# Kernel optimization log

Hardware: AMD Instinct MI355X
Metric: run time of the kernel (lower is better)

## Reference

```python
import jax, jax.numpy as jnp
import numpy as np

H = 4          # attention heads
NEG_SLOPE = 0.2

def _gat_layer(h, src, dst, W, a_src, a_dst, b):
    # h: [N, F_in]; W: [F_in, H*D]; a_src/a_dst: [H, D]; b: [D]
    N = h.shape[0]
    D = a_src.shape[1]
    xh = (h @ W).reshape(N, H, D)                       # [N,H,D]
    al_src = jnp.einsum('nhd,hd->nh', xh, a_src)        # [N,H]
    al_dst = jnp.einsum('nhd,hd->nh', xh, a_dst)        # [N,H]
    e = jax.nn.leaky_relu(al_src[src] + al_dst[dst], NEG_SLOPE)  # [E,H]
    # segment softmax over incoming edges of each destination node
    m = jax.ops.segment_max(e, dst, num_segments=N)     # [N,H]
    ex = jnp.exp(e - m[dst])
    s = jax.ops.segment_sum(ex, dst, num_segments=N)
    alpha = ex / (s[dst] + 1e-16)                       # [E,H]
    out = jax.ops.segment_sum(xh[src] * alpha[:, :, None], dst, num_segments=N)  # [N,H,D]
    return out.mean(axis=1) + b                         # concat=False -> mean heads


def setup_inputs() -> dict:
    key = jax.random.key(0)
    ks = jax.random.split(key, 16)
    N, E, F_in, Dh = 50000, 400000, 128, 128
    inp = {
        'x': jax.random.normal(ks[0], (N, F_in), jnp.float32),
        'edge_index': jax.random.randint(ks[1], (2, E), 0, N, jnp.int64),
    }
    def glorot(k, shape):
        fan = shape[0] + shape[-1]
        return jax.random.uniform(k, shape, jnp.float32, -1.0, 1.0) * np.sqrt(6.0 / fan)
    dims = [F_in, Dh, Dh]
    for i, fin in enumerate(dims, start=1):
        inp[f'W{i}'] = glorot(ks[2 + 4 * i], (fin, H * Dh))
        inp[f'a_src{i}'] = glorot(ks[3 + 4 * i], (H, Dh))
        inp[f'a_dst{i}'] = glorot(ks[4 + 4 * i], (H, Dh))
        inp[f'b{i}'] = jnp.zeros((Dh,), jnp.float32)
    inp['Wp'] = glorot(ks[2], (Dh, Dh))
    inp['bp'] = jnp.zeros((Dh,), jnp.float32)
    return inp


def reference(x, edge_index, W1, a_src1, a_dst1, b1, W2, a_src2, a_dst2, b2,
              W3, a_src3, a_dst3, b3, Wp, bp):
    N = x.shape[0]
    loops = jnp.arange(N, dtype=edge_index.dtype)
    src = jnp.concatenate([edge_index[0], loops])   # GATConv adds self-loops
    dst = jnp.concatenate([edge_index[1], loops])
    h = x
    for W, a_s, a_d, b in ((W1, a_src1, a_dst1, b1),
                           (W2, a_src2, a_dst2, b2),
                           (W3, a_src3, a_dst3, b3)):
        h = _gat_layer(h, src, dst, W, a_s, a_d, b)
        h = jax.nn.relu(h)   # dropout is identity in eval mode
    return h @ Wp + bp
```

## Files before the change

### kernel.cpp

```cpp
#include <hip/hip_runtime.h>
#include <cstddef>
#include <cstdint>

typedef _Float16 half8 __attribute__((ext_vector_type(8)));
typedef float f32x4 __attribute__((ext_vector_type(4)));
typedef float f32x2 __attribute__((ext_vector_type(2)));
typedef unsigned short ushort_t;
typedef unsigned int uint_t;
typedef ushort_t ushort4v __attribute__((ext_vector_type(4)));
typedef float f32x4v __attribute__((ext_vector_type(4)));

#define INV_LN2 1.4426950408889634f

__device__ __forceinline__ ushort_t f_to_f16(float f) {
  _Float16 h = (_Float16)f;
  union { _Float16 h; ushort_t u; } v; v.h = h; return v.u;
}
__device__ __forceinline__ float f16_to_f(ushort_t u) {
  union { ushort_t u; _Float16 h; } v; v.u = u; return (float)v.h;
}

__global__ __launch_bounds__(64) void detect_i64_kernel(const int* __restrict__ ei,
                                                        int* __restrict__ flag) {
  if (threadIdx.x == 0) {
    int is32 = 0;
    for (int i = 1; i < 1001; i += 2) {
      if (ei[i] != 0) { is32 = 1; break; }
    }
    *flag = is32;
  }
}

__device__ __forceinline__ int load_src(const int* ei, int is32, int E, int e) {
  return is32 ? ei[e] : ei[2 * e];
}
__device__ __forceinline__ int load_dst(const int* ei, int is32, int E, int e) {
  return is32 ? ei[E + e] : ei[2 * (E + e)];
}

__global__ __launch_bounds__(256) void deg_kernel(const int* __restrict__ ei,
                                                  const int* __restrict__ flag,
                                                  int E, int N, int* __restrict__ deg) {
  int e = blockIdx.x * 256 + threadIdx.x;
  if (e >= E + N) return;
  int d = (e < E) ? load_dst(ei, *flag, E, e) : (e - E);
  atomicAdd(&deg[d], 1);
}

__global__ __launch_bounds__(256) void scan_blk_kernel(const int* __restrict__ deg,
                                                       int* __restrict__ rowptr,
                                                       int* __restrict__ bsum, int N) {
  __shared__ int buf[256];
  int b = blockIdx.x, t = threadIdx.x, i = b * 256 + t;
  int v = (i < N) ? deg[i] : 0;
  buf[t] = v;
  __syncthreads();
  for (int off = 1; off < 256; off <<= 1) {
    int add = (t >= off) ? buf[t - off] : 0;
    __syncthreads();
    buf[t] += add;
    __syncthreads();
  }
  if (i < N) rowptr[i + 1] = buf[t];
  if (t == 255) bsum[b] = buf[255];
  if (b == 0 && t == 0) rowptr[0] = 0;
}

__global__ __launch_bounds__(256) void scan_top_kernel(int* __restrict__ bsum, int NB) {
  __shared__ int buf[256];
  int t = threadIdx.x;
  int v = (t < NB) ? bsum[t] : 0;
  buf[t] = v;
  __syncthreads();
  for (int off = 1; off < 256; off <<= 1) {
    int add = (t >= off) ? buf[t - off] : 0;
    __syncthreads();
    buf[t] += add;
    __syncthreads();
  }
  if (t < NB) bsum[t] = buf[t];
}

__global__ __launch_bounds__(256) void scan_add_kernel(int* __restrict__ rowptr,
                                                       const int* __restrict__ bsum, int N) {
  int b = blockIdx.x, t = threadIdx.x, i = b * 256 + t;
  if (b > 0 && i < N) rowptr[i + 1] += bsum[b - 1];
}

__global__ __launch_bounds__(256) void fill_kernel(const int* __restrict__ ei,
                                                   const int* __restrict__ flag,
                                                   int E, int N,
                                                   const int* __restrict__ rowptr,
                                                   int* __restrict__ fillc,
                                                   int* __restrict__ colbuf) {
  int e = blockIdx.x * 256 + threadIdx.x;
  if (e >= E + N) return;
  int s, d;
  if (e < E) { int is32 = *flag; s = load_src(ei, is32, E, e); d = load_dst(ei, is32, E, e); }
  else { s = e - E; d = s; }
  int pos = atomicAdd(&fillc[d], 1);
  colbuf[rowptr[d] + pos] = s;
}

__global__ __launch_bounds__(256) void split_x16_kernel(const float* __restrict__ h,
                                                        ushort_t* __restrict__ h16,
                                                        int n) {
  int i = (blockIdx.x * 256 + threadIdx.x) * 4;
  if (i >= n) return;
  f32x4v v = *(const f32x4v*)&h[i];
  ushort4v s;
  s[0] = f_to_f16(v[0]); s[1] = f_to_f16(v[1]);
  s[2] = f_to_f16(v[2]); s[3] = f_to_f16(v[3]);
  *(ushort4v*)&h16[i] = s;
}

__global__ __launch_bounds__(256) void split_wt_frag_kernel(const float* __restrict__ W,
                                                            ushort_t* __restrict__ Wf) {
  int t = blockIdx.x * 256 + threadIdx.x;
  int blk = t >> 7, rem = t & 127;
  int c16 = blk >> 4, k8 = blk & 15;
  int cl = rem >> 3, kl = rem & 7;
  int col = c16 * 16 + cl, k = k8 * 8 + kl;
  Wf[t] = f_to_f16(W[(size_t)k * 128 + col]);
}

__global__ __launch_bounds__(256) void split_wstack_frag_kernel(const float* __restrict__ W,
                                                                ushort_t* __restrict__ Wf) {
  int t = blockIdx.x * 256 + threadIdx.x;
  int c16 = t >> 13;
  int r = t & 8191;
  int k8 = r >> 7;
  int rem = r & 127;
  int rl = rem >> 3, kl = rem & 7;
  int col = c16 * 16 + rl;
  int k = k8 * 8 + kl;
  int h = k >> 7, f = k & 127;
  Wf[t] = f_to_f16(0.25f * W[(size_t)f * 512 + h * 128 + col]);
}

__global__ __launch_bounds__(256) void wsd_kernel(const float* __restrict__ W,
                                                  const float* __restrict__ a_src,
                                                  const float* __restrict__ a_dst,
                                                  float* __restrict__ Ws4,
                                                  float* __restrict__ Wd4,
                                                  float* __restrict__ Wsh,
                                                  float* __restrict__ Wdh) {
  int wave = threadIdx.x >> 6, lane = threadIdx.x & 63;
  int f = blockIdx.x * 4 + wave;
  int base = lane * 8;
  float4 w0 = *(const float4*)&W[(size_t)f * 512 + base];
  float4 w1 = *(const float4*)&W[(size_t)f * 512 + base + 4];
  float4 s0 = *(const float4*)&a_src[base];
  float4 s1 = *(const float4*)&a_src[base + 4];
  float4 d0 = *(const float4*)&a_dst[base];
  float4 d1 = *(const float4*)&a_dst[base + 4];
  float ps = w0.x*s0.x + w0.y*s0.y + w0.z*s0.z + w0.w*s0.w
           + w1.x*s1.x + w1.y*s1.y + w1.z*s1.z + w1.w*s1.w;
  float pd = w0.x*d0.x + w0.y*d0.y + w0.z*d0.z + w0.w*d0.w
           + w1.x*d1.x + w1.y*d1.y + w1.z*d1.z + w1.w*d1.w;
#pragma unroll
  for (int off = 1; off <= 8; off <<= 1) {
    ps += __shfl_xor(ps, off);
    pd += __shfl_xor(pd, off);
  }
  if ((lane & 15) == 0) {
    int h = lane >> 4;
    float vs = ps * INV_LN2, vd = pd * INV_LN2;
    Ws4[f * 4 + h] = vs;
    Wd4[f * 4 + h] = vd;
    Wsh[h * 128 + f] = vs;
    Wdh[h * 128 + f] = vd;
  }
}

__global__ __launch_bounds__(256) void al_x_kernel(const float* __restrict__ x,
                                                   const float* __restrict__ Wsh,
                                                   const float* __restrict__ Wdh,
                                                   float* __restrict__ al_src,
                                                   float* __restrict__ al_dst, int N) {
  __shared__ float sWs[512], sWd[512];
  int t = threadIdx.x;
  sWs[t] = Wsh[t]; sWs[t + 256] = Wsh[t + 256];
  sWd[t] = Wdh[t]; sWd[t + 256] = Wdh[t + 256];
  __syncthreads();
  int wave = t >> 6, lane = t & 63;
  int n = blockIdx.x * 4 + wave;
  if (n >= N) return;
  float2 hv = *(const float2*)&x[(size_t)n * 128 + lane * 2];
  float p[8];
#pragma unroll
  for (int hh = 0; hh < 4; ++hh) {
    p[hh]     = hv.x * sWs[hh * 128 + 2 * lane] + hv.y * sWs[hh * 128 + 2 * lane + 1];
    p[4 + hh] = hv.x * sWd[hh * 128 + 2 * lane] + hv.y * sWd[hh * 128 + 2 * lane + 1];
  }
#pragma unroll
  for (int off = 32; off; off >>= 1)
#pragma unroll
    for (int i = 0; i < 8; ++i) p[i] += __shfl_xor(p[i], off);
  if (lane == 0) {
#pragma unroll
    for (int hh = 0; hh < 4; ++hh) {
      al_src[n * 4 + hh] = p[hh];
      al_dst[n * 4 + hh] = p[4 + hh];
    }
  }
}

__global__ __launch_bounds__(256) void agg_G_kernel(const ushort_t* __restrict__ h16,
                                                    const float* __restrict__ al_src,
                                                    const float* __restrict__ al_dst,
                                                    const int* __restrict__ rowptr,
                                                    const int* __restrict__ colbuf,
                                                    ushort_t* __restrict__ Gf, int N) {
  int wave = threadIdx.x >> 6, lane = threadIdx.x & 63;
  int hl = lane & 31;
  int half_base = lane & 32;
  int q = hl >> 2, hc = hl & 3;
  int qb = lane & ~3;
  int n = blockIdx.x * 8 + wave * 2 + (lane >> 5);
  bool alive = n < N;
  int beg = 0, d = 0;
  float ald_hc = 0.f;
  if (alive) {
    beg = rowptr[n];
    d = rowptr[n + 1] - beg;
    ald_hc = al_dst[(size_t)n * 4 + hc];
  }
  int dm1 = max(d - 1, 0);
  float m_run = -1e30f;
  f32x2 ss01 = {0.f, 0.f}, ss23 = {0.f, 0.f};
  f32x2 a0a = {0.f,0.f}, a0b = {0.f,0.f};
  f32x2 a1a = {0.f,0.f}, a1b = {0.f,0.f};
  f32x2 a2a = {0.f,0.f}, a2b = {0.f,0.f};
  f32x2 a3a = {0.f,0.f}, a3b = {0.f,0.f};

  for (int c0 = 0; c0 < d; c0 += 8) {
    int cn = min(8, d - c0);
    int j = c0 + q;
    int sq = colbuf[beg + min(j, dm1)];
    float e = al_src[(size_t)sq * 4 + hc] + ald_hc;
    e = fmaxf(e, 0.2f * e);
    e = (q < cn) ? e : -1e30f;
    float mc = e;
    mc = fmaxf(mc, __shfl_xor(mc, 4));
    mc = fmaxf(mc, __shfl_xor(mc, 8));
    mc = fmaxf(mc, __shfl_xor(mc, 16));
    float nm = fmaxf(m_run, mc);
    float fown = exp2f(m_run - nm);
    m_run = nm;
    float w_own = (q < cn) ? exp2f(e - nm) : 0.f;
    float f0 = __shfl(fown, qb + 0), f1 = __shfl(fown, qb + 1);
    float f2 = __shfl(fown, qb + 2), f3 = __shfl(fown, qb + 3);
    ss01 *= f32x2{f0, f1}; ss23 *= f32x2{f2, f3};
    f32x2 F0 = {f0, f0}, F1 = {f1, f1}, F2 = {f2, f2}, F3 = {f3, f3};
    a0a *= F0; a0b *= F0; a1a *= F1; a1b *= F1;
    a2a *= F2; a2b *= F2; a3a *= F3; a3b *= F3;
    int s_c = __shfl(sq, half_base);
    ushort4v hv_c = *(const ushort4v*)&h16[(size_t)s_c * 128 + hl * 4];
    for (int jj = 0; jj < cn; ++jj) {
      int s_n = __shfl(sq, half_base + min(jj + 1, cn - 1) * 4);
      ushort4v hv_n = *(const ushort4v*)&h16[(size_t)s_n * 128 + hl * 4];
      int wb = half_base + jj * 4;
      float w0 = __shfl(w_own, wb + 0);
      float w1 = __shfl(w_own, wb + 1);
      float w2 = __shfl(w_own, wb + 2);
      float w3 = __shfl(w_own, wb + 3);
      ss01 += f32x2{w0, w1}; ss23 += f32x2{w2, w3};
      f32x2 v01 = {f16_to_f(hv_c[0]), f16_to_f(hv_c[1])};
      f32x2 v23 = {f16_to_f(hv_c[2]), f16_to_f(hv_c[3])};
      a0a += f32x2{w0, w0} * v01; a0b += f32x2{w0, w0} * v23;
      a1a += f32x2{w1, w1} * v01; a1b += f32x2{w1, w1} * v23;
      a2a += f32x2{w2, w2} * v01; a2b += f32x2{w2, w2} * v23;
      a3a += f32x2{w3, w3} * v01; a3b += f32x2{w3, w3} * v23;
      hv_c = hv_n;
    }
  }
  if (!alive) return;
  float g[4][4];
  float inv;
  inv = 1.f / (ss01.x + 1e-16f);
  g[0][0] = a0a.x * inv; g[0][1] = a0a.y * inv; g[0][2] = a0b.x * inv; g[0][3] = a0b.y * inv;
  inv = 1.f / (ss01.y + 1e-16f);
  g[1][0] = a1a.x * inv; g[1][1] = a1a.y * inv; g[1][2] = a1b.x * inv; g[1][3] = a1b.y * inv;
  inv = 1.f / (ss23.x + 1e-16f);
  g[2][0] = a2a.x * inv; g[2][1] = a2a.y * inv; g[2][2] = a2b.x * inv; g[2][3] = a2b.y * inv;
  inv = 1.f / (ss23.y + 1e-16f);
  g[3][0] = a3a.x * inv; g[3][1] = a3a.y * inv; g[3][2] = a3b.x * inv; g[3][3] = a3b.y * inv;
#pragma unroll
  for (int h = 0; h < 4; ++h) {
    ushort_t q0 = f_to_f16(g[h][0]), q1 = f_to_f16(g[h][1]);
    ushort_t q2 = f_to_f16(g[h][2]), q3 = f_to_f16(g[h][3]);
    size_t o = ((size_t)(n >> 4) * 64 + h * 16 + (hl >> 1)) * 128 + (n & 15) * 8 + (hl & 1) * 4;
    *(uint2*)&Gf[o] = make_uint2((uint_t)q0 | ((uint_t)q1 << 16),
                                 (uint_t)q2 | ((uint_t)q3 << 16));
  }
}

template <int K, int MODE>
__global__ __launch_bounds__(256) void gemm_frag_kernel(
    const ushort_t* __restrict__ Af, const ushort_t* __restrict__ Bf,
    ushort_t* __restrict__ H16, ushort_t* __restrict__ Cf16, float* __restrict__ Cf,
    const float* __restrict__ WsN, const float* __restrict__ WdN,
    float* __restrict__ alS, float* __restrict__ alD,
    int M, const float* __restrict__ bias) {
  constexpr int KT = K >> 5;
  constexpr int PS = 16 * K;
  int lane = threadIdx.x & 63;
  int wid = blockIdx.x * 4 + (threadIdx.x >> 6);
  int krow = lane >> 4, ml = lane & 15;
  int lb = krow * 128 + ml * 8;
  size_t abase = (size_t)wid * PS + lb;
  f32x4 acc[8] = {};
  half8 a_c = *(const half8*)&Af[abase];
#pragma unroll
  for (int kt = 0; kt < KT; ++kt) {
    half8 a_n = a_c;
    if (kt + 1 < KT) a_n = *(const half8*)&Af[abase + (kt + 1) * 512];
    half8 b[8];
#pragma unroll
    for (int j = 0; j < 8; ++j)
      b[j] = *(const half8*)&Bf[j * PS + kt * 512 + lb];
#pragma unroll
    for (int j = 0; j < 8; ++j)
      acc[j] = __builtin_amdgcn_mfma_f32_16x16x32_f16(a_c, b[j], acc[j], 0, 0, 0);
    a_c = a_n;
  }
  int wrow0 = wid * 16;
  if (MODE == 0) {
    float ps[4][4] = {};
    float pd[4][4] = {};
#pragma unroll
    for (int j = 0; j < 8; ++j) {
      int col = j * 16 + ml;
      float bv = bias[col];
      float4 w4s = *(const float4*)&WsN[col * 4];
      float4 w4d = *(const float4*)&WdN[col * 4];
#pragma unroll
      for (int r = 0; r < 4; ++r) {
        int row = wrow0 + krow * 4 + r;
        float v = fmaxf(acc[j][r] + bv, 0.f);
        if (row < M) H16[(size_t)row * 128 + col] = f_to_f16(v);
        ps[0][r] += v * w4s.x; ps[1][r] += v * w4s.y;
        ps[2][r] += v * w4s.z; ps[3][r] += v * w4s.w;
        pd[0][r] += v * w4d.x; pd[1][r] += v * w4d.y;
        pd[2][r] += v * w4d.z; pd[3][r] += v * w4d.w;
      }
    }
#pragma unroll
    for (int off = 1; off <= 8; off <<= 1) {
#pragma unroll
      for (int hh = 0; hh < 4; ++hh)
#pragma unroll
        for (int r = 0; r < 4; ++r) {
          ps[hh][r] += __shfl_xor(ps[hh][r], off);
          pd[hh][r] += __shfl_xor(pd[hh][r], off);
        }
    }
    if (ml == 0) {
#pragma unroll
      for (int r = 0; r < 4; ++r) {
        int row = wrow0 + krow * 4 + r;
        if (row < M) {
#pragma unroll
          for (int hh = 0; hh < 4; ++hh) {
            alS[row * 4 + hh] = ps[hh][r];
            alD[row * 4 + hh] = pd[hh][r];
          }
        }
      }
    }
  } else {
#pragma unroll
    for (int j = 0; j < 8; ++j) {
      int col = j * 16 + ml;
      float bv = bias[col];
#pragma unroll
      for (int r = 0; r < 4; ++r) {
        int row = wrow0 + krow * 4 + r;
        if (row < M) {
          float v = acc[j][r] + bv;
          if (MODE != 2) v = fmaxf(v, 0.f);
          if (MODE == 1) {
            size_t o = ((size_t)(row >> 4) * 16 + (col >> 3)) * 128 + (row & 15) * 8 + (col & 7);
            Cf16[o] = f_to_f16(v);
          } else {
            Cf[(size_t)row * 128 + col] = v;
          }
        }
      }
    }
  }
}

extern "C" void kernel_launch(void* const* d_in, const int* in_sizes, int n_in,
                              void* d_out, int out_size, void* d_ws, size_t ws_size,
                              hipStream_t stream) {
  const float* x  = (const float*)d_in[0];
  const int*   ei = (const int*)d_in[1];
  const float* Wl[3]  = {(const float*)d_in[2], (const float*)d_in[6], (const float*)d_in[10]};
  const float* asr[3] = {(const float*)d_in[3], (const float*)d_in[7], (const float*)d_in[11]};
  const float* adr[3] = {(const float*)d_in[4], (const float*)d_in[8], (const float*)d_in[12]};
  const float* bl[3]  = {(const float*)d_in[5], (const float*)d_in[9], (const float*)d_in[13]};
  const float* Wp = (const float*)d_in[14];
  const float* bp = (const float*)d_in[15];

  const int N = in_sizes[0] / 128;
  const int E = in_sizes[1] / 2;
  const int EN = E + N;
  const int Mtiles = (N + 127) / 128;
  const int Mp = Mtiles * 128;
  const int NB = (N + 255) / 256;
  const int NPB = Mp / 16 / 4;

  char* ws = (char*)d_ws;
  size_t off = 0;
  auto carve = [&](size_t bytes) -> void* {
    void* p = ws + off;
    off = (off + bytes + 255) & ~(size_t)255;
    return p;
  };
  ushort_t* Gf    = (ushort_t*)carve((size_t)Mp * 512 * 2);
  ushort_t* h16   = (ushort_t*)carve((size_t)N * 128 * 2);
  ushort_t* h3f   = (ushort_t*)carve((size_t)Mp * 128 * 2);
  ushort_t* wsf   = (ushort_t*)carve((size_t)128 * 512 * 2);
  float*    alsrc = (float*)carve((size_t)N * 4 * 4);
  float*    aldst = (float*)carve((size_t)N * 4 * 4);
  float*    Ws4   = (float*)carve(3 * 512 * 4);
  float*    Wd4   = (float*)carve(3 * 512 * 4);
  float*    Wsh   = (float*)carve(3 * 512 * 4);
  float*    Wdh   = (float*)carve(3 * 512 * 4);
  int*      rowptr= (int*)carve((size_t)(N + 1) * 4);
  int*      deg   = (int*)carve((size_t)N * 4);
  int*      bsum  = (int*)carve(256 * 4);
  int*      fillc = (int*)carve((size_t)N * 4);
  int*      colbuf= (int*)carve((size_t)EN * 4);
  int*      flag  = (int*)carve(256);

  detect_i64_kernel<<<1, 64, 0, stream>>>(ei, flag);
  hipMemsetAsync(deg, 0, (size_t)N * 4, stream);
  hipMemsetAsync(fillc, 0, (size_t)N * 4, stream);
  int ebl = (EN + 255) / 256;
  deg_kernel<<<ebl, 256, 0, stream>>>(ei, flag, E, N, deg);
  scan_blk_kernel<<<NB, 256, 0, stream>>>(deg, rowptr, bsum, N);
  scan_top_kernel<<<1, 256, 0, stream>>>(bsum, NB);
  scan_add_kernel<<<NB, 256, 0, stream>>>(rowptr, bsum, N);
  fill_kernel<<<ebl, 256, 0, stream>>>(ei, flag, E, N, rowptr, fillc, colbuf);

  const int n_real = N * 128;
  split_x16_kernel<<<(n_real / 4 + 255) / 256, 256, 0, stream>>>(x, h16, n_real);
  for (int L = 0; L < 3; ++L)
    wsd_kernel<<<32, 256, 0, stream>>>(Wl[L], asr[L], adr[L],
                                       Ws4 + L * 512, Wd4 + L * 512,
                                       Wsh + L * 512, Wdh + L * 512);
  al_x_kernel<<<(N + 3) / 4, 256, 0, stream>>>(x, Wsh, Wdh, alsrc, aldst, N);

  for (int L = 0; L < 3; ++L) {
    agg_G_kernel<<<Mp / 8, 256, 0, stream>>>(h16, alsrc, aldst,
                                             rowptr, colbuf, Gf, N);
    split_wstack_frag_kernel<<<256, 256, 0, stream>>>(Wl[L], wsf);
    if (L < 2) {
      gemm_frag_kernel<512, 0><<<NPB, 256, 0, stream>>>(Gf, wsf,
                                                        h16, nullptr, nullptr,
                                                        Ws4 + (L + 1) * 512, Wd4 + (L + 1) * 512,
                                                        alsrc, aldst, N, bl[L]);
    } else {
      gemm_frag_kernel<512, 1><<<NPB, 256, 0, stream>>>(Gf, wsf,
                                                        nullptr, h3f, nullptr,
                                                        nullptr, nullptr, nullptr, nullptr,
                                                        N, bl[L]);
    }
  }

  split_wt_frag_kernel<<<64, 256, 0, stream>>>(Wp, wsf);
  gemm_frag_kernel<128, 2><<<NPB, 256, 0, stream>>>(h3f, wsf,
                                                    nullptr, nullptr, (float*)d_out,
                                                    nullptr, nullptr, nullptr, nullptr,
                                                    N, bp);
}
```

Measured before the change: 329.6 us.

## Split GEMM K-loop across wave pairs with LDS reduction and batch weight prep

```diff
diff --git a/kernel.cpp b/kernel.cpp
--- a/kernel.cpp
+++ b/kernel.cpp
@@ -114,28 +114,34 @@
   *(ushort4v*)&h16[i] = s;
 }
 
-__global__ __launch_bounds__(256) void split_wt_frag_kernel(const float* __restrict__ W,
-                                                            ushort_t* __restrict__ Wf) {
-  int t = blockIdx.x * 256 + threadIdx.x;
-  int blk = t >> 7, rem = t & 127;
-  int c16 = blk >> 4, k8 = blk & 15;
-  int cl = rem >> 3, kl = rem & 7;
-  int col = c16 * 16 + cl, k = k8 * 8 + kl;
-  Wf[t] = f_to_f16(W[(size_t)k * 128 + col]);
-}
-
-__global__ __launch_bounds__(256) void split_wstack_frag_kernel(const float* __restrict__ W,
-                                                                ushort_t* __restrict__ Wf) {
-  int t = blockIdx.x * 256 + threadIdx.x;
-  int c16 = t >> 13;
-  int r = t & 8191;
-  int k8 = r >> 7;
-  int rem = r & 127;
-  int rl = rem >> 3, kl = rem & 7;
-  int col = c16 * 16 + rl;
-  int k = k8 * 8 + kl;
-  int h = k >> 7, f = k & 127;
-  Wf[t] = f_to_f16(0.25f * W[(size_t)f * 512 + h * 128 + col]);
+__global__ __launch_bounds__(256) void prep_weights_kernel(
+    const float* __restrict__ W0, const float* __restrict__ W1,
+    const float* __restrict__ W2, const float* __restrict__ Wp,
+    ushort_t* __restrict__ wsf0, ushort_t* __restrict__ wsf1,
+    ushort_t* __restrict__ wsf2, ushort_t* __restrict__ wpf) {
+  int b = blockIdx.x;
+  if (b < 768) {
+    int L = b >> 8;
+    const float* W = (L == 0) ? W0 : (L == 1) ? W1 : W2;
+    ushort_t* out = (L == 0) ? wsf0 : (L == 1) ? wsf1 : wsf2;
+    int t = (b & 255) * 256 + threadIdx.x;
+    int c16 = t >> 13;
+    int r = t & 8191;
+    int k8 = r >> 7;
+    int rem = r & 127;
+    int rl = rem >> 3, kl = rem & 7;
+    int col = c16 * 16 + rl;
+    int k = k8 * 8 + kl;
+    int h = k >> 7, f = k & 127;
+    out[t] = f_to_f16(0.25f * W[(size_t)f * 512 + h * 128 + col]);
+  } else {
+    int t = (b - 768) * 256 + threadIdx.x;
+    int blk = t >> 7, rem = t & 127;
+    int c16 = blk >> 4, k8 = blk & 15;
+    int cl = rem >> 3, kl = rem & 7;
+    int col = c16 * 16 + cl, k = k8 * 8 + kl;
+    wpf[t] = f_to_f16(Wp[(size_t)k * 128 + col]);
+  }
 }
 
 __global__ __launch_bounds__(256) void wsd_kernel(const float* __restrict__ W,
@@ -304,27 +310,54 @@
     float* __restrict__ alS, float* __restrict__ alD,
     int M, const float* __restrict__ bias) {
   constexpr int KT = K >> 5;
+  constexpr int KTH = KT >> 1;
   constexpr int PS = 16 * K;
+  __shared__ float lacc[2][8][4][64];
   int lane = threadIdx.x & 63;
-  int wid = blockIdx.x * 4 + (threadIdx.x >> 6);
+  int wv = threadIdx.x >> 6;
+  int pair = wv >> 1, khalf = wv & 1;
+  int wid = blockIdx.x * 2 + pair;
   int krow = lane >> 4, ml = lane & 15;
   int lb = krow * 128 + ml * 8;
-  size_t abase = (size_t)wid * PS + lb;
+  size_t abase = (size_t)wid * PS + lb + (size_t)khalf * KTH * 512;
+  size_t bbase = (size_t)lb + (size_t)khalf * KTH * 512;
   f32x4 acc[8] = {};
   half8 a_c = *(const half8*)&Af[abase];
-#pragma unroll
-  for (int kt = 0; kt < KT; ++kt) {
+  half8 b_c[8];
+#pragma unroll
+  for (int j = 0; j < 8; ++j) b_c[j] = *(const half8*)&Bf[j * PS + bbase];
+#pragma unroll
+  for (int kt = 0; kt < KTH; ++kt) {
     half8 a_n = a_c;
-    if (kt + 1 < KT) a_n = *(const half8*)&Af[abase + (kt + 1) * 512];
-    half8 b[8];
+    half8 b_n[8];
+#pragma unroll
+    for (int j = 0; j < 8; ++j) b_n[j] = b_c[j];
+    if (kt + 1 < KTH) {
+      a_n = *(const half8*)&Af[abase + (kt + 1) * 512];
+#pragma unroll
+      for (int j = 0; j < 8; ++j)
+        b_n[j] = *(const half8*)&Bf[j * PS + bbase + (kt + 1) * 512];
+    }
 #pragma unroll
     for (int j = 0; j < 8; ++j)
-      b[j] = *(const half8*)&Bf[j * PS + kt * 512 + lb];
+      acc[j] = __builtin_amdgcn_mfma_f32_16x16x32_f16(a_c, b_c[j], acc[j], 0, 0, 0);
+    a_c = a_n;
+#pragma unroll
+    for (int j = 0; j < 8; ++j) b_c[j] = b_n[j];
+  }
+  if (khalf == 1) {
 #pragma unroll
     for (int j = 0; j < 8; ++j)
-      acc[j] = __builtin_amdgcn_mfma_f32_16x16x32_f16(a_c, b[j], acc[j], 0, 0, 0);
-    a_c = a_n;
-  }
+#pragma unroll
+      for (int c = 0; c < 4; ++c) lacc[pair][j][c][lane] = acc[j][c];
+  }
+  __syncthreads();
+  if (khalf == 1) return;
+#pragma unroll
+  for (int j = 0; j < 8; ++j)
+#pragma unroll
+    for (int c = 0; c < 4; ++c) acc[j][c] += lacc[pair][j][c][lane];
+
   int wrow0 = wid * 16;
   if (MODE == 0) {
     float ps[4][4] = {};
@@ -410,7 +443,7 @@
   const int Mtiles = (N + 127) / 128;
   const int Mp = Mtiles * 128;
   const int NB = (N + 255) / 256;
-  const int NPB = Mp / 16 / 4;
+  const int NPB2 = Mp / 16 / 2;
 
   char* ws = (char*)d_ws;
   size_t off = 0;
@@ -422,7 +455,10 @@
   ushort_t* Gf    = (ushort_t*)carve((size_t)Mp * 512 * 2);
   ushort_t* h16   = (ushort_t*)carve((size_t)N * 128 * 2);
   ushort_t* h3f   = (ushort_t*)carve((size_t)Mp * 128 * 2);
-  ushort_t* wsf   = (ushort_t*)carve((size_t)128 * 512 * 2);
+  ushort_t* wsf0  = (ushort_t*)carve((size_t)128 * 512 * 2);
+  ushort_t* wsf1  = (ushort_t*)carve((size_t)128 * 512 * 2);
+  ushort_t* wsf2  = (ushort_t*)carve((size_t)128 * 512 * 2);
+  ushort_t* wpf   = (ushort_t*)carve((size_t)128 * 128 * 2);
   float*    alsrc = (float*)carve((size_t)N * 4 * 4);
   float*    aldst = (float*)carve((size_t)N * 4 * 4);
   float*    Ws4   = (float*)carve(3 * 512 * 4);
@@ -448,32 +484,33 @@
 
   const int n_real = N * 128;
   split_x16_kernel<<<(n_real / 4 + 255) / 256, 256, 0, stream>>>(x, h16, n_real);
+  prep_weights_kernel<<<832, 256, 0, stream>>>(Wl[0], Wl[1], Wl[2], Wp,
+                                               wsf0, wsf1, wsf2, wpf);
   for (int L = 0; L < 3; ++L)
     wsd_kernel<<<32, 256, 0, stream>>>(Wl[L], asr[L], adr[L],
                                        Ws4 + L * 512, Wd4 + L * 512,
                                        Wsh + L * 512, Wdh + L * 512);
   al_x_kernel<<<(N + 3) / 4, 256, 0, stream>>>(x, Wsh, Wdh, alsrc, aldst, N);
 
+  ushort_t* wsfL[3] = {wsf0, wsf1, wsf2};
   for (int L = 0; L < 3; ++L) {
     agg_G_kernel<<<Mp / 8, 256, 0, stream>>>(h16, alsrc, aldst,
                                              rowptr, colbuf, Gf, N);
-    split_wstack_frag_kernel<<<256, 256, 0, stream>>>(Wl[L], wsf);
     if (L < 2) {
-      gemm_frag_kernel<512, 0><<<NPB, 256, 0, stream>>>(Gf, wsf,
-                                                        h16, nullptr, nullptr,
-                                                        Ws4 + (L + 1) * 512, Wd4 + (L + 1) * 512,
-                                                        alsrc, aldst, N, bl[L]);
+      gemm_frag_kernel<512, 0><<<NPB2, 256, 0, stream>>>(Gf, wsfL[L],
+                                                         h16, nullptr, nullptr,
+                                                         Ws4 + (L + 1) * 512, Wd4 + (L + 1) * 512,
+                                                         alsrc, aldst, N, bl[L]);
     } else {
-      gemm_frag_kernel<512, 1><<<NPB, 256, 0, stream>>>(Gf, wsf,
-                                                        nullptr, h3f, nullptr,
-                                                        nullptr, nullptr, nullptr, nullptr,
-                                                        N, bl[L]);
-    }
-  }
-
-  split_wt_frag_kernel<<<64, 256, 0, stream>>>(Wp, wsf);
-  gemm_frag_kernel<128, 2><<<NPB, 256, 0, stream>>>(h3f, wsf,
-                                                    nullptr, nullptr, (float*)d_out,
-                                                    nullptr, nullptr, nullptr, nullptr,
-                                                    N, bp);
-}
+      gemm_frag_kernel<512, 1><<<NPB2, 256, 0, stream>>>(Gf, wsfL[L],
+                                                         nullptr, h3f, nullptr,
+                                                         nullptr, nullptr, nullptr, nullptr,
+                                                         N, bl[L]);
+    }
+  }
+
+  gemm_frag_kernel<128, 2><<<NPB2, 256, 0, stream>>>(h3f, wpf,
+                                                     nullptr, nullptr, (float*)d_out,
+                                                     nullptr, nullptr, nullptr, nullptr,
+                                                     N, bp);
+}
```

Result: faster. 312.8 us (-5.1%).
